# Performance work log

Hardware: AMD Instinct MI355X
Metric: run time of the kernel (lower is better)

Reference implementation:

```python
import jax, jax.numpy as jnp
import numpy as np
from jax import lax

B, H, W, CIN = 16, 96, 320, 32
N_ACTIVE = 200000
COUT = 256
FC_IN = (H // 8) * (W // 8) * 128  # 12*40*128 = 61440


def _conv(x, w, b):
    # stride-2, pad-1, 3x3 conv in NCHW / OIHW layout
    y = lax.conv_general_dilated(x, w, (2, 2), [(1, 1), (1, 1)],
                                 dimension_numbers=('NCHW', 'OIHW', 'NCHW'))
    return y + b[None, :, None, None]


def _maxpool3(x):
    # 3x3 maxpool, stride 1, pad 1 (NCHW)
    return lax.reduce_window(x, -jnp.inf, lax.max,
                             (1, 1, 3, 3), (1, 1, 1, 1),
                             [(0, 0), (0, 0), (1, 1), (1, 1)])


def setup_inputs() -> dict:
    key = jax.random.key(0)
    ks = jax.random.split(key, 12)
    input_feat = jax.random.normal(ks[0], (B, H, W, CIN), dtype=jnp.float32)
    cb = jax.random.randint(ks[1], (N_ACTIVE, 1), 0, B)
    cy = jax.random.randint(ks[2], (N_ACTIVE, 1), 0, H)
    cx = jax.random.randint(ks[3], (N_ACTIVE, 1), 0, W)
    spconv_coords = jnp.concatenate([cb, cy, cx], axis=1).astype(jnp.int32)
    w1 = jax.random.normal(ks[4], (32, CIN, 3, 3), dtype=jnp.float32) * (1.0 / np.sqrt(CIN * 9))
    b1 = jax.random.normal(ks[5], (32,), dtype=jnp.float32) * 0.01
    w2 = jax.random.normal(ks[6], (64, 32, 3, 3), dtype=jnp.float32) * (1.0 / np.sqrt(32 * 9))
    b2 = jax.random.normal(ks[7], (64,), dtype=jnp.float32) * 0.01
    w3 = jax.random.normal(ks[8], (128, 64, 3, 3), dtype=jnp.float32) * (1.0 / np.sqrt(64 * 9))
    b3 = jax.random.normal(ks[9], (128,), dtype=jnp.float32) * 0.01
    fc_w = jax.random.normal(ks[10], (COUT, FC_IN), dtype=jnp.float32) * (1.0 / np.sqrt(FC_IN))
    fc_b = jax.random.normal(ks[11], (COUT,), dtype=jnp.float32) * 0.01
    return {"input_feat": input_feat, "spconv_coords": spconv_coords,
            "w1": w1, "b1": b1, "w2": w2, "b2": b2, "w3": w3, "b3": b3,
            "fc_w": fc_w, "fc_b": fc_b}


def reference(input_feat, spconv_coords, w1, b1, w2, b2, w3, b3, fc_w, fc_b):
    bi = spconv_coords[:, 0]
    yi = spconv_coords[:, 1]
    xi = spconv_coords[:, 2]
    # gather active-site features, then scatter into a dense NHWC grid
    feats = input_feat[bi, yi, xi]                       # [N, CIN]
    dense = jnp.zeros_like(input_feat).at[bi, yi, xi].set(feats)
    x = dense.transpose(0, 3, 1, 2)                      # [B, CIN, H, W]
    x = jax.nn.relu(_maxpool3(_conv(x, w1, b1)))         # [B, 32, H/2, W/2]
    x = jax.nn.relu(_maxpool3(_conv(x, w2, b2)))         # [B, 64, H/4, W/4]
    x = jax.nn.relu(_maxpool3(_conv(x, w3, b3)))         # [B, 128, H/8, W/8]
    x = x.reshape(x.shape[0], -1)                        # [B, FC_IN]
    return jax.nn.relu(x @ fc_w.T + fc_b)                # [B, COUT]
```

## Files before the change

### kernel.cpp

```cpp
#include <hip/hip_runtime.h>

#define NB 16
#define NH 96
#define NW 320
#define NCIN 32

typedef __attribute__((ext_vector_type(8))) short short8;
typedef __attribute__((ext_vector_type(4))) float f32x4;

__device__ inline unsigned short f2bf(float f) {
    union { float f; unsigned int u; } v; v.f = f;
    unsigned int r = v.u + 0x7FFF + ((v.u >> 16) & 1);
    return (unsigned short)(r >> 16);
}

__device__ inline unsigned int pack_bf2(float a, float b) {
    unsigned int ua = __float_as_uint(a), ub = __float_as_uint(b);
    return (ub & 0xFFFF0000u) | (ua >> 16);
}

__global__ void scatter_mask(const int* __restrict__ coords, unsigned char* __restrict__ mask, int n) {
    int i = blockIdx.x * blockDim.x + threadIdx.x;
    if (i < n) {
        int b = coords[i * 3 + 0];
        int y = coords[i * 3 + 1];
        int x = coords[i * 3 + 2];
        mask[(b * NH + y) * NW + x] = 1;
    }
}

__global__ __launch_bounds__(256) void prep_wfrag(const float* __restrict__ w1,
                                                  const float* __restrict__ w2,
                                                  const float* __restrict__ w3,
                                                  unsigned short* __restrict__ f1,
                                                  unsigned short* __restrict__ f2,
                                                  unsigned short* __restrict__ f3) {
    int i = blockIdx.x * blockDim.x + threadIdx.x;
    if (i < 9216) {
        int j = i & 7, lane = (i >> 3) & 63, nt = (i >> 9) & 1, tap = i >> 10;
        int ic = ((lane >> 4) * 8) + j, oc = nt * 16 + (lane & 15);
        f1[i] = f2bf(w1[(oc * 32 + ic) * 9 + tap]);
    } else if (i < 27648) {
        int v = i - 9216;
        int j = v & 7, lane = (v >> 3) & 63, nt = (v >> 9) & 3, tap = v >> 11;
        int ic = ((lane >> 4) * 8) + j, oc = nt * 16 + (lane & 15);
        f2[v] = f2bf(w2[(oc * 32 + ic) * 9 + tap]);
    } else if (i < 101376) {
        int v = i - 27648;
        int j = v & 7, lane = (v >> 3) & 63, nt = (v >> 9) & 7, kk = v >> 12;
        int tap = kk >> 1, ks = kk & 1;
        int ic = ks * 32 + ((lane >> 4) * 8) + j, oc = nt * 16 + (lane & 15);
        f3[v] = f2bf(w3[(oc * 64 + ic) * 9 + tap]);
    }
}

template<int IC, int OC, int NL, int IH, int IW, int OH, int OW, bool FP32IN>
__global__ __launch_bounds__(256) void conv_mfma(
    const void* __restrict__ inPtr,
    const unsigned short* __restrict__ wfrag,
    const float* __restrict__ bias,
    const unsigned char* __restrict__ mask,
    float* __restrict__ out)
{
    constexpr int KS = IC / 32;
    constexpr int NT = OC / 16;
    constexpr int NG = NT / NL;
    constexpr int NSTRIPS = NB * OH * OW / 16;

    const int wid  = (blockIdx.x * 256 + threadIdx.x) >> 6;
    const int lane = threadIdx.x & 63;
    const int ntb  = (wid % NG) * NL;
    const int s    = wid / NG;
    if (s >= NSTRIPS) return;
    const int quad = lane >> 4;
    const int lm   = lane & 15;

    const int p0 = s * 16;
    const int posA = p0 + lm;
    const int b  = posA / (OH * OW);
    const int rr = posA % (OH * OW);
    const int oy = rr / OW, ox = rr % OW;
    const int iy0 = oy * 2 - 1, ix0 = ox * 2 - 1;

    int cell[9];
    bool okb[9];
    #pragma unroll
    for (int t9 = 0; t9 < 9; t9++) {
        const int iy = iy0 + t9 / 3;
        const int ix = ix0 + t9 % 3;
        const bool ok = (iy >= 0) && (iy < IH) && (ix >= 0) && (ix < IW);
        cell[t9] = ok ? ((b * IH + iy) * IW + ix) : 0;
        okb[t9] = ok;
    }

    short8 zero8;
    #pragma unroll
    for (int j = 0; j < 8; j++) zero8[j] = 0;

    f32x4 acc[NL][2];
    #pragma unroll
    for (int nl = 0; nl < NL; nl++)
        #pragma unroll
        for (int pp = 0; pp < 2; pp++)
            acc[nl][pp] = (f32x4){0.f, 0.f, 0.f, 0.f};

    #pragma unroll 1
    for (int ks = 0; ks < KS; ks++) {
        short8 av[9];
        if (FP32IN) {
            unsigned char mk[9];
            #pragma unroll
            for (int t9 = 0; t9 < 9; t9++) mk[t9] = mask[cell[t9]];
            #pragma unroll
            for (int t9 = 0; t9 < 9; t9++) {
                const float4* ap = (const float4*)((const float*)inPtr + (long)cell[t9] * IC + quad * 8);
                float4 v0 = ap[0], v1 = ap[1];
                union { short8 s8; unsigned int u[4]; } tt;
                tt.u[0] = pack_bf2(v0.x, v0.y);
                tt.u[1] = pack_bf2(v0.z, v0.w);
                tt.u[2] = pack_bf2(v1.x, v1.y);
                tt.u[3] = pack_bf2(v1.z, v1.w);
                bool ok = okb[t9] && (mk[t9] != 0);
                av[t9] = ok ? tt.s8 : zero8;
            }
        } else {
            #pragma unroll
            for (int t9 = 0; t9 < 9; t9++) {
                short8 v = *(const short8*)((const unsigned short*)inPtr + (long)cell[t9] * IC + ks * 32 + quad * 8);
                av[t9] = okb[t9] ? v : zero8;
            }
        }
        #pragma unroll
        for (int nl = 0; nl < NL; nl++) {
            #pragma unroll
            for (int t9 = 0; t9 < 9; t9++) {
                short8 bf = *(const short8*)(wfrag + (((t9 * KS + ks) * NT + ntb + nl) * 64 + lane) * 8);
                if (t9 & 1) acc[nl][1] = __builtin_amdgcn_mfma_f32_16x16x32_bf16(av[t9], bf, acc[nl][1], 0, 0, 0);
                else        acc[nl][0] = __builtin_amdgcn_mfma_f32_16x16x32_bf16(av[t9], bf, acc[nl][0], 0, 0, 0);
            }
        }
    }

    const long rowBase = (long)p0 + quad * 4;
    #pragma unroll
    for (int nl = 0; nl < NL; nl++) {
        const int oc = (ntb + nl) * 16 + lm;
        const float bv = bias[oc];
        #pragma unroll
        for (int reg = 0; reg < 4; reg++)
            out[(rowBase + reg) * OC + oc] = acc[nl][0][reg] + acc[nl][1][reg] + bv;
    }
}

template<int C, int HH, int WW, bool BF16OUT>
__global__ __launch_bounds__(256) void maxpool3_relu(const float* __restrict__ in, void* __restrict__ outv) {
    constexpr int C4 = C / 4;
    int i = blockIdx.x * blockDim.x + threadIdx.x;
    if (i >= NB * HH * WW * C4) return;
    int c = i % C4;
    int x = (i / C4) % WW;
    int y = (i / (C4 * WW)) % HH;
    int b = i / (C4 * WW * HH);
    float4 m = make_float4(-3.0e38f, -3.0e38f, -3.0e38f, -3.0e38f);
    #pragma unroll
    for (int dy = -1; dy <= 1; dy++) {
        int yy = y + dy;
        if (yy < 0 || yy >= HH) continue;
        #pragma unroll
        for (int dx = -1; dx <= 1; dx++) {
            int xx = x + dx;
            if (xx < 0 || xx >= WW) continue;
            float4 v = ((const float4*)in)[((b * HH + yy) * WW + xx) * C4 + c];
            m.x = fmaxf(m.x, v.x);
            m.y = fmaxf(m.y, v.y);
            m.z = fmaxf(m.z, v.z);
            m.w = fmaxf(m.w, v.w);
        }
    }
    m.x = fmaxf(m.x, 0.f);
    m.y = fmaxf(m.y, 0.f);
    m.z = fmaxf(m.z, 0.f);
    m.w = fmaxf(m.w, 0.f);
    if (BF16OUT) {
        ushort4 o;
        o.x = f2bf(m.x); o.y = f2bf(m.y); o.z = f2bf(m.z); o.w = f2bf(m.w);
        ((ushort4*)outv)[i] = o;
    } else {
        ((float4*)outv)[i] = m;
    }
}

__global__ __launch_bounds__(256) void transpose_fc(const float* __restrict__ in, float* __restrict__ xT) {
    __shared__ float tile_s[32 * 16 * 17];
    const int pt = blockIdx.x % 30;
    const int ct = blockIdx.x / 30;
    const int pos0 = pt * 16, c0 = ct * 32;
    const int t = threadIdx.x;
    {
        const int b = t / 16, pl = t % 16;
        const float4* src = (const float4*)(in + ((long)(b * 480 + pos0 + pl)) * 128 + c0);
        #pragma unroll
        for (int q = 0; q < 8; q++) {
            float4 v = src[q];
            tile_s[((4 * q + 0) * 16 + pl) * 17 + b] = v.x;
            tile_s[((4 * q + 1) * 16 + pl) * 17 + b] = v.y;
            tile_s[((4 * q + 2) * 16 + pl) * 17 + b] = v.z;
            tile_s[((4 * q + 3) * 16 + pl) * 17 + b] = v.w;
        }
    }
    __syncthreads();
    {
        const int w = t / 64, l = t % 64;
        const int pl2 = l / 4, b4 = l % 4;
        #pragma unroll
        for (int i = 0; i < 8; i++) {
            int cl = w + 4 * i;
            const float* ls = &tile_s[(cl * 16 + pl2) * 17 + 4 * b4];
            float4 v = make_float4(ls[0], ls[1], ls[2], ls[3]);
            *(float4*)(xT + ((long)(c0 + cl) * 480 + pos0 + pl2) * 16 + 4 * b4) = v;
        }
    }
}

__global__ __launch_bounds__(256) void fc_stage1(const float* __restrict__ xT,
                                                 const float* __restrict__ fw,
                                                 float* __restrict__ partial)
{
    __shared__ float red[32 * 257];
    const int tile  = blockIdx.x / 15;
    const int chunk = blockIdx.x % 15;
    const int t = threadIdx.x;
    const int K = 61440, KC = 4096;

    float acc[4][16];
    #pragma unroll
    for (int o = 0; o < 4; o++)
        #pragma unroll
        for (int bb = 0; bb < 16; bb++) acc[o][bb] = 0.f;

    const int k0 = chunk * KC;
    #pragma unroll 2
    for (int k = k0 + t; k < k0 + KC; k += 256) {
        const float4* xp = (const float4*)(xT + (long)k * 16);
        float4 x0 = xp[0], x1 = xp[1], x2 = xp[2], x3 = xp[3];
        #pragma unroll
        for (int o = 0; o < 4; o++) {
            float w = fw[(long)(tile * 4 + o) * K + k];
            acc[o][0]  = fmaf(w, x0.x, acc[o][0]);
            acc[o][1]  = fmaf(w, x0.y, acc[o][1]);
            acc[o][2]  = fmaf(w, x0.z, acc[o][2]);
            acc[o][3]  = fmaf(w, x0.w, acc[o][3]);
            acc[o][4]  = fmaf(w, x1.x, acc[o][4]);
            acc[o][5]  = fmaf(w, x1.y, acc[o][5]);
            acc[o][6]  = fmaf(w, x1.z, acc[o][6]);
            acc[o][7]  = fmaf(w, x1.w, acc[o][7]);
            acc[o][8]  = fmaf(w, x2.x, acc[o][8]);
            acc[o][9]  = fmaf(w, x2.y, acc[o][9]);
            acc[o][10] = fmaf(w, x2.z, acc[o][10]);
            acc[o][11] = fmaf(w, x2.w, acc[o][11]);
            acc[o][12] = fmaf(w, x3.x, acc[o][12]);
            acc[o][13] = fmaf(w, x3.y, acc[o][13]);
            acc[o][14] = fmaf(w, x3.z, acc[o][14]);
            acc[o][15] = fmaf(w, x3.w, acc[o][15]);
        }
    }

    #pragma unroll
    for (int oo = 0; oo < 2; oo++)
        #pragma unroll
        for (int bb = 0; bb < 16; bb++)
            red[(oo * 16 + bb) * 257 + t] = acc[oo][bb];
    __syncthreads();
    if (t < 32) {
        float s = 0.f;
        for (int i = 0; i < 256; i++) s += red[t * 257 + i];
        partial[((long)chunk * 256 + tile * 4 + (t / 16)) * 16 + (t % 16)] = s;
    }
    __syncthreads();
    #pragma unroll
    for (int oo = 0; oo < 2; oo++)
        #pragma unroll
        for (int bb = 0; bb < 16; bb++)
            red[(oo * 16 + bb) * 257 + t] = acc[2 + oo][bb];
    __syncthreads();
    if (t < 32) {
        float s = 0.f;
        for (int i = 0; i < 256; i++) s += red[t * 257 + i];
        partial[((long)chunk * 256 + tile * 4 + 2 + (t / 16)) * 16 + (t % 16)] = s;
    }
}

__global__ __launch_bounds__(256) void fc_reduce(const float* __restrict__ partial,
                                                 const float* __restrict__ fcb,
                                                 float* __restrict__ out)
{
    int i = blockIdx.x * blockDim.x + threadIdx.x;
    if (i >= 4096) return;
    int oc = i / 16, b = i % 16;
    float s = fcb[oc];
    #pragma unroll
    for (int c = 0; c < 15; c++) s += partial[(c * 256 + oc) * 16 + b];
    out[b * 256 + oc] = fmaxf(s, 0.f);
}

extern "C" void kernel_launch(void* const* d_in, const int* in_sizes, int n_in,
                              void* d_out, int out_size, void* d_ws, size_t ws_size,
                              hipStream_t stream) {
    const float* input  = (const float*)d_in[0];
    const int*   coords = (const int*)d_in[1];
    const float* w1 = (const float*)d_in[2];
    const float* b1 = (const float*)d_in[3];
    const float* w2 = (const float*)d_in[4];
    const float* b2 = (const float*)d_in[5];
    const float* w3 = (const float*)d_in[6];
    const float* b3 = (const float*)d_in[7];
    const float* fcw = (const float*)d_in[8];
    const float* fcb = (const float*)d_in[9];
    float* outp = (float*)d_out;

    const int n_active = in_sizes[1] / 3;

    char* ws = (char*)d_ws;
    unsigned short* wf1 = (unsigned short*)ws;
    unsigned short* wf2 = wf1 + 9216;
    unsigned short* wf3 = wf2 + 18432;
    unsigned char*  mask = (unsigned char*)(ws + 204800);
    char* regA = ws + 204800 + 491520;
    char* regB = regA + 15728640;
    float* partial = (float*)(regB + 7864320);

    float*          conv1o  = (float*)regA;
    unsigned short* pool1bf = (unsigned short*)regB;
    float*          conv2o  = (float*)regA;
    unsigned short* pool2bf = (unsigned short*)regB;
    float*          conv3o  = (float*)regA;
    float*          pool3f  = (float*)regB;
    float*          xT      = (float*)regA;

    hipMemsetAsync(mask, 0, NB * NH * NW, stream);
    prep_wfrag<<<396, 256, 0, stream>>>(w1, w2, w3, wf1, wf2, wf3);
    scatter_mask<<<(n_active + 255) / 256, 256, 0, stream>>>(coords, mask, n_active);

    conv_mfma<32, 32, 2, 96, 320, 48, 160, true>
        <<<1920, 256, 0, stream>>>(input, wf1, b1, mask, conv1o);
    maxpool3_relu<32, 48, 160, true><<<3840, 256, 0, stream>>>(conv1o, pool1bf);

    conv_mfma<32, 64, 2, 48, 160, 24, 80, false>
        <<<960, 256, 0, stream>>>(pool1bf, wf2, b2, nullptr, conv2o);
    maxpool3_relu<64, 24, 80, true><<<1920, 256, 0, stream>>>(conv2o, pool2bf);

    conv_mfma<64, 128, 2, 24, 80, 12, 40, false>
        <<<480, 256, 0, stream>>>(pool2bf, wf3, b3, nullptr, conv3o);
    maxpool3_relu<128, 12, 40, false><<<960, 256, 0, stream>>>(conv3o, pool3f);

    transpose_fc<<<120, 256, 0, stream>>>(pool3f, xT);
    fc_stage1<<<960, 256, 0, stream>>>(xT, fcw, partial);
    fc_reduce<<<16, 256, 0, stream>>>(partial, fcb, outp);
}
```

Measured before the change: 248.4 us.

## Scatter active sites into a bf16 dense grid instead of masking fp32 input in conv1

Replaces the byte mask plus in-conv fp32 load/convert/mask with a pre-pass that zeroes a dense bf16 grid and scatters only active-site features (converted to bf16) into it. The scatter is fused with weight-fragment prep into one setup kernel. Conv1 then reads bf16 directly like the later convs, halving its input bytes and removing mask loads. In exchange it adds a large memset of the bf16 grid and scatter traffic.

Result: no change. 246.8 us (-0.6%).

```diff
diff --git a/kernel.cpp b/kernel.cpp
--- a/kernel.cpp
+++ b/kernel.cpp
@@ -14,52 +14,54 @@
     return (unsigned short)(r >> 16);
 }
 
-__device__ inline unsigned int pack_bf2(float a, float b) {
-    unsigned int ua = __float_as_uint(a), ub = __float_as_uint(b);
-    return (ub & 0xFFFF0000u) | (ua >> 16);
-}
-
-__global__ void scatter_mask(const int* __restrict__ coords, unsigned char* __restrict__ mask, int n) {
-    int i = blockIdx.x * blockDim.x + threadIdx.x;
-    if (i < n) {
-        int b = coords[i * 3 + 0];
-        int y = coords[i * 3 + 1];
-        int x = coords[i * 3 + 2];
-        mask[(b * NH + y) * NW + x] = 1;
-    }
-}
-
-__global__ __launch_bounds__(256) void prep_wfrag(const float* __restrict__ w1,
-                                                  const float* __restrict__ w2,
-                                                  const float* __restrict__ w3,
-                                                  unsigned short* __restrict__ f1,
-                                                  unsigned short* __restrict__ f2,
-                                                  unsigned short* __restrict__ f3) {
-    int i = blockIdx.x * blockDim.x + threadIdx.x;
-    if (i < 9216) {
-        int j = i & 7, lane = (i >> 3) & 63, nt = (i >> 9) & 1, tap = i >> 10;
-        int ic = ((lane >> 4) * 8) + j, oc = nt * 16 + (lane & 15);
-        f1[i] = f2bf(w1[(oc * 32 + ic) * 9 + tap]);
-    } else if (i < 27648) {
-        int v = i - 9216;
-        int j = v & 7, lane = (v >> 3) & 63, nt = (v >> 9) & 3, tap = v >> 11;
-        int ic = ((lane >> 4) * 8) + j, oc = nt * 16 + (lane & 15);
-        f2[v] = f2bf(w2[(oc * 32 + ic) * 9 + tap]);
-    } else if (i < 101376) {
-        int v = i - 27648;
-        int j = v & 7, lane = (v >> 3) & 63, nt = (v >> 9) & 7, kk = v >> 12;
-        int tap = kk >> 1, ks = kk & 1;
-        int ic = ks * 32 + ((lane >> 4) * 8) + j, oc = nt * 16 + (lane & 15);
-        f3[v] = f2bf(w3[(oc * 64 + ic) * 9 + tap]);
-    }
-}
-
-template<int IC, int OC, int NL, int IH, int IW, int OH, int OW, bool FP32IN>
+__global__ __launch_bounds__(256) void setup_all(const float* __restrict__ w1,
+                                                 const float* __restrict__ w2,
+                                                 const float* __restrict__ w3,
+                                                 unsigned short* __restrict__ f1,
+                                                 unsigned short* __restrict__ f2,
+                                                 unsigned short* __restrict__ f3,
+                                                 const int* __restrict__ coords,
+                                                 const float* __restrict__ input,
+                                                 unsigned short* __restrict__ inBf,
+                                                 int n) {
+    if (blockIdx.x < 396) {
+        int i = blockIdx.x * 256 + threadIdx.x;
+        if (i < 9216) {
+            int j = i & 7, lane = (i >> 3) & 63, nt = (i >> 9) & 1, tap = i >> 10;
+            int ic = ((lane >> 4) * 8) + j, oc = nt * 16 + (lane & 15);
+            f1[i] = f2bf(w1[(oc * 32 + ic) * 9 + tap]);
+        } else if (i < 27648) {
+            int v = i - 9216;
+            int j = v & 7, lane = (v >> 3) & 63, nt = (v >> 9) & 3, tap = v >> 11;
+            int ic = ((lane >> 4) * 8) + j, oc = nt * 16 + (lane & 15);
+            f2[v] = f2bf(w2[(oc * 32 + ic) * 9 + tap]);
+        } else if (i < 101376) {
+            int v = i - 27648;
+            int j = v & 7, lane = (v >> 3) & 63, nt = (v >> 9) & 7, kk = v >> 12;
+            int tap = kk >> 1, ks = kk & 1;
+            int ic = ks * 32 + ((lane >> 4) * 8) + j, oc = nt * 16 + (lane & 15);
+            f3[v] = f2bf(w3[(oc * 64 + ic) * 9 + tap]);
+        }
+    } else {
+        int i = (blockIdx.x - 396) * 256 + threadIdx.x;
+        if (i >= n * 4) return;
+        int ci = i >> 2, q = i & 3;
+        int b = coords[ci * 3 + 0], y = coords[ci * 3 + 1], x = coords[ci * 3 + 2];
+        long base = ((long)((b * NH + y) * NW + x)) * NCIN + q * 8;
+        const float4* src = (const float4*)(input + base);
+        float4 v0 = src[0], v1 = src[1];
+        union { short8 s8; unsigned short us[8]; } o;
+        o.us[0] = f2bf(v0.x); o.us[1] = f2bf(v0.y); o.us[2] = f2bf(v0.z); o.us[3] = f2bf(v0.w);
+        o.us[4] = f2bf(v1.x); o.us[5] = f2bf(v1.y); o.us[6] = f2bf(v1.z); o.us[7] = f2bf(v1.w);
+        *(short8*)(inBf + base) = o.s8;
+    }
+}
+
+template<int IC, int OC, int NL, int IH, int IW, int OH, int OW>
 __global__ __launch_bounds__(256) void conv_mfma(
-    const void* __restrict__ inPtr,
+    const unsigned short* __restrict__ inPtr,
     const unsigned short* __restrict__ wfrag,
     const float* __restrict__ bias,
-    const unsigned char* __restrict__ mask,
     float* __restrict__ out)
 {
     constexpr int KS = IC / 32;
@@ -107,28 +109,10 @@
     #pragma unroll 1
     for (int ks = 0; ks < KS; ks++) {
         short8 av[9];
-        if (FP32IN) {
-            unsigned char mk[9];
-            #pragma unroll
-            for (int t9 = 0; t9 < 9; t9++) mk[t9] = mask[cell[t9]];
-            #pragma unroll
-            for (int t9 = 0; t9 < 9; t9++) {
-                const float4* ap = (const float4*)((const float*)inPtr + (long)cell[t9] * IC + quad * 8);
-                float4 v0 = ap[0], v1 = ap[1];
-                union { short8 s8; unsigned int u[4]; } tt;
-                tt.u[0] = pack_bf2(v0.x, v0.y);
-                tt.u[1] = pack_bf2(v0.z, v0.w);
-                tt.u[2] = pack_bf2(v1.x, v1.y);
-                tt.u[3] = pack_bf2(v1.z, v1.w);
-                bool ok = okb[t9] && (mk[t9] != 0);
-                av[t9] = ok ? tt.s8 : zero8;
-            }
-        } else {
-            #pragma unroll
-            for (int t9 = 0; t9 < 9; t9++) {
-                short8 v = *(const short8*)((const unsigned short*)inPtr + (long)cell[t9] * IC + ks * 32 + quad * 8);
-                av[t9] = okb[t9] ? v : zero8;
-            }
+        #pragma unroll
+        for (int t9 = 0; t9 < 9; t9++) {
+            short8 v = *(const short8*)(inPtr + (long)cell[t9] * IC + ks * 32 + quad * 8);
+            av[t9] = okb[t9] ? v : zero8;
         }
         #pragma unroll
         for (int nl = 0; nl < NL; nl++) {
@@ -324,8 +308,8 @@
     unsigned short* wf1 = (unsigned short*)ws;
     unsigned short* wf2 = wf1 + 9216;
     unsigned short* wf3 = wf2 + 18432;
-    unsigned char*  mask = (unsigned char*)(ws + 204800);
-    char* regA = ws + 204800 + 491520;
+    unsigned short* inBf = (unsigned short*)(ws + 204800);
+    char* regA = ws + 204800 + 31457280;
     char* regB = regA + 15728640;
     float* partial = (float*)(regB + 7864320);
 
@@ -337,20 +321,21 @@
     float*          pool3f  = (float*)regB;
     float*          xT      = (float*)regA;
 
-    hipMemsetAsync(mask, 0, NB * NH * NW, stream);
-    prep_wfrag<<<396, 256, 0, stream>>>(w1, w2, w3, wf1, wf2, wf3);
-    scatter_mask<<<(n_active + 255) / 256, 256, 0, stream>>>(coords, mask, n_active);
-
-    conv_mfma<32, 32, 2, 96, 320, 48, 160, true>
-        <<<1920, 256, 0, stream>>>(input, wf1, b1, mask, conv1o);
+    hipMemsetAsync(inBf, 0, 31457280, stream);
+    const int scatterBlocks = (n_active * 4 + 255) / 256;
+    setup_all<<<396 + scatterBlocks, 256, 0, stream>>>(w1, w2, w3, wf1, wf2, wf3,
+                                                       coords, input, inBf, n_active);
+
+    conv_mfma<32, 32, 2, 96, 320, 48, 160>
+        <<<1920, 256, 0, stream>>>(inBf, wf1, b1, conv1o);
     maxpool3_relu<32, 48, 160, true><<<3840, 256, 0, stream>>>(conv1o, pool1bf);
 
-    conv_mfma<32, 64, 2, 48, 160, 24, 80, false>
-        <<<960, 256, 0, stream>>>(pool1bf, wf2, b2, nullptr, conv2o);
+    conv_mfma<32, 64, 2, 48, 160, 24, 80>
+        <<<960, 256, 0, stream>>>(pool1bf, wf2, b2, conv2o);
     maxpool3_relu<64, 24, 80, true><<<1920, 256, 0, stream>>>(conv2o, pool2bf);
 
-    conv_mfma<64, 128, 2, 24, 80, 12, 40, false>
-        <<<480, 256, 0, stream>>>(pool2bf, wf3, b3, nullptr, conv3o);
+    conv_mfma<64, 128, 2, 24, 80, 12, 40>
+        <<<480, 256, 0, stream>>>(pool2bf, wf3, b3, conv3o);
     maxpool3_relu<128, 12, 40, false><<<960, 256, 0, stream>>>(conv3o, pool3f);
 
     transpose_fc<<<120, 256, 0, stream>>>(pool3f, xT);
```
